# Kernel optimization log

Hardware: AMD Instinct MI355X
Metric: run time of the kernel (lower is better)

Reference implementation:

```python
import jax, jax.numpy as jnp
import numpy as np

N = 50000      # nodes
E = 800000     # directed edges (before self loops)
IN = 64        # in_channels
HID = 96       # hidden_dim
HEADS = 4
C = HID // HEADS
L = 4          # num_layers
G = 1024       # num graphs (molecules)
OUT = 1
BN_EPS = 1e-5


def setup_inputs() -> dict:
    key = jax.random.key(0)
    ks = jax.random.split(key, 20)
    x = jax.random.normal(ks[0], (N, IN), jnp.float32)
    edge_index = jax.random.randint(ks[1], (2, E), 0, N, dtype=jnp.int32)
    batch = jnp.sort(jax.random.randint(ks[2], (N,), 0, G, dtype=jnp.int32))
    def lin(k, fi, fo):
        return jax.random.normal(k, (fi, fo), jnp.float32) / np.sqrt(fi)
    return {
        "x": x, "edge_index": edge_index, "batch": batch,
        "W_in": lin(ks[3], IN, HID), "b_in": jnp.zeros((HID,), jnp.float32),
        "Wg": jax.random.normal(ks[4], (L, HID, HID), jnp.float32) / np.sqrt(HID),
        "att_src": jax.random.normal(ks[5], (L, HEADS, C), jnp.float32) / np.sqrt(C),
        "att_dst": jax.random.normal(ks[6], (L, HEADS, C), jnp.float32) / np.sqrt(C),
        "bg": jnp.zeros((L, HID), jnp.float32),
        "gamma": jnp.ones((L, HID), jnp.float32),
        "beta": jnp.zeros((L, HID), jnp.float32),
        "rm": 0.1 * jax.random.normal(ks[7], (L, HID), jnp.float32),
        "rv": jax.random.uniform(ks[8], (L, HID), jnp.float32, 0.5, 1.5),
        "W_jk": lin(ks[9], HID * L, HID), "b_jk": jnp.zeros((HID,), jnp.float32),
        "W_h1": lin(ks[10], HID, HID), "b_h1": jnp.zeros((HID,), jnp.float32),
        "W_h2": lin(ks[11], HID, OUT), "b_h2": jnp.zeros((OUT,), jnp.float32),
    }


def gat_conv(h_in, src, dst, W, a_s, a_d, b):
    # PyG GATConv (concat=True, negative_slope=0.2), eval mode (no dropout)
    h = (h_in @ W).reshape(N, HEADS, C)                      # [N,H,C]
    e = (h * a_s).sum(-1)[src] + (h * a_d).sum(-1)[dst]      # [E',H]
    e = jax.nn.leaky_relu(e, 0.2)
    m = jax.ops.segment_max(e, dst, num_segments=N)          # segment softmax over dst
    p = jnp.exp(e - m[dst])
    z = jax.ops.segment_sum(p, dst, num_segments=N)
    alpha = p / (z[dst] + 1e-16)                             # [E',H]
    out = jax.ops.segment_sum(h[src] * alpha[:, :, None], dst, num_segments=N)
    return out.reshape(N, HID) + b


def reference(x, edge_index, batch, W_in, b_in, Wg, att_src, att_dst, bg,
              gamma, beta, rm, rv, W_jk, b_jk, W_h1, b_h1, W_h2, b_h2):
    # add self loops (PyG GATConv default)
    loops = jnp.arange(N, dtype=edge_index.dtype)
    src = jnp.concatenate([edge_index[0], loops])
    dst = jnp.concatenate([edge_index[1], loops])

    h = jax.nn.elu(x @ W_in + b_in)
    pooled = []
    for i in range(L):
        hn = gat_conv(h, src, dst, Wg[i], att_src[i], att_dst[i], bg[i])
        hn = (hn - rm[i]) / jnp.sqrt(rv[i] + BN_EPS) * gamma[i] + beta[i]
        h = h + jax.nn.elu(hn)                               # residual
        pooled.append(jax.ops.segment_sum(h, batch, num_segments=G))
    z = jax.nn.elu(jnp.concatenate(pooled, axis=-1) @ W_jk + b_jk)  # JK
    z = jax.nn.relu(z @ W_h1 + b_h1)
    return z @ W_h2 + b_h2                                    # [G, OUT]
```

## Files before the change

kernel.cpp:

```cpp
#include <hip/hip_runtime.h>
#include <hip/hip_bf16.h>
#include <math.h>

#define NODES 50000
#define EDGES 800000
#define EP    850000
#define INCH  64
#define HIDD  96
#define NHEAD 4
#define CHD   24
#define NLAY  4
#define NGRF  1024
#define BNEPS 1e-5f
#define NB    49
#define HSTR  98

__device__ __forceinline__ float elu1(float v) { return v > 0.f ? v : __expf(v) - 1.f; }

__device__ __forceinline__ unsigned short f2bf(float f) {
    unsigned u = __float_as_uint(f);
    return (unsigned short)((u + 0x7fffu + ((u >> 16) & 1u)) >> 16);
}

__device__ __forceinline__ float rl_f(float v, int l) {
    return __int_as_float(__builtin_amdgcn_readlane(__float_as_int(v), l));
}

__device__ __forceinline__ float bnorm(float a, const float* __restrict__ bg,
                                       const float* __restrict__ rm, const float* __restrict__ rv,
                                       const float* __restrict__ gamma, const float* __restrict__ beta,
                                       int ch) {
    float hn = a + bg[ch];
    return (hn - rm[ch]) / sqrtf(rv[ch] + BNEPS) * gamma[ch] + beta[ch];
}

__device__ __forceinline__ void edge_sd(int e, const int* __restrict__ S,
                                        const int* __restrict__ D, int& s, int& d) {
    if (e < EDGES) { s = S[e]; d = D[e]; } else { s = e - EDGES; d = s; }
}


__global__ __launch_bounds__(256) void k_count(const int* __restrict__ S, const int* __restrict__ D,
                                               int* __restrict__ cnt) {
    int e = blockIdx.x * blockDim.x + threadIdx.x;
    if (e >= EP) return;
    int s, d; edge_sd(e, S, D, s, d);
    atomicAdd(&cnt[d], 1);
}

__global__ __launch_bounds__(1024) void k_scan1(const int* __restrict__ cnt,
                                                int* __restrict__ off, int* __restrict__ bsum) {
    __shared__ int sd[1024];
    int t = threadIdx.x;
    int i = blockIdx.x * 1024 + t;
    int v = (i < NODES) ? cnt[i] : 0;
    sd[t] = v; __syncthreads();
    for (int o = 1; o < 1024; o <<= 1) {
        int tv = (t >= o) ? sd[t - o] : 0;
        __syncthreads();
        sd[t] += tv; __syncthreads();
    }
    if (i < NODES) off[i] = sd[t] - v;
    if (t == 1023) bsum[blockIdx.x] = sd[1023];
}

__global__ __launch_bounds__(1024) void k_scan3m(int* __restrict__ off, const int* __restrict__ bsum,
                                                 int* __restrict__ cursor) {
    int carry = 0;
    for (int b = 0; b < blockIdx.x; ++b) carry += bsum[b];
    int i = blockIdx.x * 1024 + threadIdx.x;
    if (i < NODES) {
        int o = off[i] + carry;
        off[i] = o;
        cursor[i] = o;
    }
    if (i == 0) off[NODES] = EP;
}

__global__ __launch_bounds__(256) void k_scatter(const int* __restrict__ S, const int* __restrict__ D,
                                                 int* __restrict__ cursor, int* __restrict__ csr_src) {
    int e = blockIdx.x * blockDim.x + threadIdx.x;
    if (e >= EP) return;
    int s, d; edge_sd(e, S, D, s, d);
    int pos = atomicAdd(&cursor[d], 1);
    csr_src[pos] = s;
}


__global__ __launch_bounds__(256) void k_in_proj_proj(const float* __restrict__ x,
                                                      const float* __restrict__ W_in,
                                                      const float* __restrict__ b_in,
                                                      const float* __restrict__ Wg0,
                                                      const float* __restrict__ asrc,
                                                      const float* __restrict__ adst,
                                                      float* __restrict__ h,
                                                      unsigned* __restrict__ hpb,
                                                      float* __restrict__ as_,
                                                      float* __restrict__ ad_) {
    __shared__ float Wl[HIDD * HIDD];
    __shared__ float hblk[64 * HSTR];
    int tid = threadIdx.x;
    for (int i = tid; i < INCH * HIDD / 4; i += 256)
        ((float4*)Wl)[i] = ((const float4*)W_in)[i];
    __syncthreads();

    int lane = tid & 63;
    int node = blockIdx.x * 64 + lane;
    bool valid = node < NODES;
    int head = tid >> 6;
    int cbase = head * CHD;

    {
        const float* __restrict__ xr = x + (size_t)node * INCH;
        float acc[CHD];
#pragma unroll
        for (int j = 0; j < CHD; ++j) acc[j] = b_in[cbase + j];
        if (valid) {
            for (int k0 = 0; k0 < INCH; k0 += 4) {
                float4 xv = *(const float4*)(xr + k0);
                const float xvv[4] = {xv.x, xv.y, xv.z, xv.w};
#pragma unroll
                for (int kk = 0; kk < 4; ++kk) {
#pragma unroll
                    for (int j4 = 0; j4 < CHD; j4 += 4) {
                        float4 wv = *(const float4*)(&Wl[(k0 + kk) * HIDD + cbase + j4]);
                        acc[j4 + 0] = fmaf(xvv[kk], wv.x, acc[j4 + 0]);
                        acc[j4 + 1] = fmaf(xvv[kk], wv.y, acc[j4 + 1]);
                        acc[j4 + 2] = fmaf(xvv[kk], wv.z, acc[j4 + 2]);
                        acc[j4 + 3] = fmaf(xvv[kk], wv.w, acc[j4 + 3]);
                    }
                }
            }
        }
        float* hrow = h + (size_t)node * HIDD + cbase;
#pragma unroll
        for (int j = 0; j < CHD; ++j) {
            float hv = elu1(acc[j]);
            hblk[lane * HSTR + cbase + j] = hv;
            if (valid) hrow[j] = hv;
        }
    }
    __syncthreads();
    for (int i = tid; i < HIDD * HIDD / 4; i += 256)
        ((float4*)Wl)[i] = ((const float4*)Wg0)[i];
    __syncthreads();

    const float* __restrict__ hr = &hblk[lane * HSTR];
    float acc[CHD] = {};
    for (int k0 = 0; k0 < HIDD; k0 += 2) {
        float2 hv = *(const float2*)(hr + k0);
        const float hvv[2] = {hv.x, hv.y};
#pragma unroll
        for (int kk = 0; kk < 2; ++kk) {
#pragma unroll
            for (int j4 = 0; j4 < CHD; j4 += 4) {
                float4 wv = *(const float4*)(&Wl[(k0 + kk) * HIDD + cbase + j4]);
                acc[j4 + 0] = fmaf(hvv[kk], wv.x, acc[j4 + 0]);
                acc[j4 + 1] = fmaf(hvv[kk], wv.y, acc[j4 + 1]);
                acc[j4 + 2] = fmaf(hvv[kk], wv.z, acc[j4 + 2]);
                acc[j4 + 3] = fmaf(hvv[kk], wv.w, acc[j4 + 3]);
            }
        }
    }
    if (valid) {
        unsigned* orow = hpb + (size_t)node * (HIDD / 2) + cbase / 2;
#pragma unroll
        for (int j = 0; j < CHD; j += 2)
            orow[j / 2] = (unsigned)f2bf(acc[j]) | ((unsigned)f2bf(acc[j + 1]) << 16);
        const float* __restrict__ s = asrc + head * CHD;
        const float* __restrict__ d = adst + head * CHD;
        float sa = 0.f, da = 0.f;
#pragma unroll
        for (int j = 0; j < CHD; ++j) { sa = fmaf(acc[j], s[j], sa); da = fmaf(acc[j], d[j], da); }
        as_[node * NHEAD + head] = sa;
        ad_[node * NHEAD + head] = da;
    }
}


__global__ __launch_bounds__(256) void k_proj(const float* __restrict__ h,
                                              const float* __restrict__ W,
                                              const float* __restrict__ asrc,
                                              const float* __restrict__ adst,
                                              unsigned* __restrict__ hpb,
                                              float* __restrict__ as_,
                                              float* __restrict__ ad_) {
    __shared__ float Wl[HIDD * HIDD];
    int tid = threadIdx.x;
    for (int i = tid; i < HIDD * HIDD / 4; i += 256)
        ((float4*)Wl)[i] = ((const float4*)W)[i];
    __syncthreads();

    int node = blockIdx.x * 64 + (tid & 63);
    if (node >= NODES) return;
    int head = tid >> 6;
    int cbase = head * CHD;
    const float* __restrict__ hr = h + (size_t)node * HIDD;

    float acc[CHD] = {};
    for (int k0 = 0; k0 < HIDD; k0 += 4) {
        float4 hv = *(const float4*)(hr + k0);
        const float hvv[4] = {hv.x, hv.y, hv.z, hv.w};
#pragma unroll
        for (int kk = 0; kk < 4; ++kk) {
#pragma unroll
            for (int j4 = 0; j4 < CHD; j4 += 4) {
                float4 wv = *(const float4*)(&Wl[(k0 + kk) * HIDD + cbase + j4]);
                acc[j4 + 0] = fmaf(hvv[kk], wv.x, acc[j4 + 0]);
                acc[j4 + 1] = fmaf(hvv[kk], wv.y, acc[j4 + 1]);
                acc[j4 + 2] = fmaf(hvv[kk], wv.z, acc[j4 + 2]);
                acc[j4 + 3] = fmaf(hvv[kk], wv.w, acc[j4 + 3]);
            }
        }
    }
    unsigned* orow = hpb + (size_t)node * (HIDD / 2) + cbase / 2;
#pragma unroll
    for (int j = 0; j < CHD; j += 2)
        orow[j / 2] = (unsigned)f2bf(acc[j]) | ((unsigned)f2bf(acc[j + 1]) << 16);

    const float* __restrict__ s = asrc + head * CHD;
    const float* __restrict__ d = adst + head * CHD;
    float sa = 0.f, da = 0.f;
#pragma unroll
    for (int j = 0; j < CHD; ++j) { sa = fmaf(acc[j], s[j], sa); da = fmaf(acc[j], d[j], da); }
    as_[node * NHEAD + head] = sa;
    ad_[node * NHEAD + head] = da;
}


__global__ __launch_bounds__(256) void k_edge(const int* __restrict__ off,
                                              const int* __restrict__ csr,
                                              const float* __restrict__ as_,
                                              const float* __restrict__ ad_,
                                              const unsigned* __restrict__ hpb,
                                              const float* __restrict__ bg,
                                              const float* __restrict__ gamma,
                                              const float* __restrict__ beta,
                                              const float* __restrict__ rm,
                                              const float* __restrict__ rv,
                                              float* __restrict__ h,
                                              const int* __restrict__ batch,
                                              float* __restrict__ pooled) {
    __shared__ float plds[512];
    int tid = threadIdx.x;
    int lane = tid & 63;
    int n0 = __builtin_amdgcn_readfirstlane(blockIdx.x * 8 + (tid >> 6) * 2);
    int n1 = n0 + 1;
    int beg0 = off[n0], end0 = off[n0 + 1], end1 = off[n0 + 2];
    int beg1 = end0;

    int hd = lane & 3, slot = lane >> 2;
    float adv0 = ad_[n0 * NHEAD + hd];
    float adv1 = ad_[n1 * NHEAD + hd];
    const int hh = (lane < 48) ? (lane / 12) : 0;
    const bool gl = (lane < 48);
    const int wb = (tid & 192) * 2;

    float a00 = 0.f, a01 = 0.f, a10 = 0.f, a11 = 0.f, zA = 0.f, zB = 0.f;
    int ca = beg0, cb = beg1;
    while (ca < end0 || cb < end1) {
        int cntA = min(16, end0 - ca);
        int cntB = min(16, end1 - cb);
        int sA = 0, sB = 0;
        if (cntA > 0) {
            int i = ca + slot, ii = min(i, end0 - 1);
            sA = csr[ii];
            float ev = as_[sA * NHEAD + hd] + adv0;
            ev = ev > 0.f ? ev : 0.2f * ev;
            float p = (i < end0) ? __expf(ev) : 0.f;
            zA += p;
            plds[wb + lane] = p;
        }
        if (cntB > 0) {
            int i = cb + slot, ii = min(i, end1 - 1);
            sB = csr[ii];
            float ev = as_[sB * NHEAD + hd] + adv1;
            ev = ev > 0.f ? ev : 0.2f * ev;
            float p = (i < end1) ? __expf(ev) : 0.f;
            zB += p;
            plds[wb + 64 + lane] = p;
        }
        if (cntA > 0) {
#pragma unroll
            for (int j = 0; j < 16; ++j) {
                if (j < cntA) {
                    int sv = __builtin_amdgcn_readlane(sA, j * 4);
                    float al = plds[wb + j * 4 + hh];
                    if (gl) {
                        unsigned u = (hpb + (size_t)sv * (HIDD / 2))[lane];
                        a00 = fmaf(__uint_as_float(u << 16),         al, a00);
                        a01 = fmaf(__uint_as_float(u & 0xffff0000u), al, a01);
                    }
                }
            }
            ca += 16;
        }
        if (cntB > 0) {
#pragma unroll
            for (int j = 0; j < 16; ++j) {
                if (j < cntB) {
                    int sv = __builtin_amdgcn_readlane(sB, j * 4);
                    float al = plds[wb + 64 + j * 4 + hh];
                    if (gl) {
                        unsigned u = (hpb + (size_t)sv * (HIDD / 2))[lane];
                        a10 = fmaf(__uint_as_float(u << 16),         al, a10);
                        a11 = fmaf(__uint_as_float(u & 0xffff0000u), al, a11);
                    }
                }
            }
            cb += 16;
        }
    }
#pragma unroll
    for (int o = 4; o < 64; o <<= 1) { zA += __shfl_xor(zA, o); zB += __shfl_xor(zB, o); }
    float za0 = rl_f(zA, 0), za1 = rl_f(zA, 1), za2 = rl_f(zA, 2), za3 = rl_f(zA, 3);
    float zb0 = rl_f(zB, 0), zb1 = rl_f(zB, 1), zb2 = rl_f(zB, 2), zb3 = rl_f(zB, 3);
    float zAl = (hh & 1) ? za1 : za0, zAh = (hh & 1) ? za3 : za2;
    float zBl = (hh & 1) ? zb1 : zb0, zBh = (hh & 1) ? zb3 : zb2;
    float zhA = (hh & 2) ? zAh : zAl;
    float zhB = (hh & 2) ? zBh : zBl;

    int g0 = batch[n0], g1 = batch[n1];
    if (gl) {
        float izA = 1.f / zhA, izB = 1.f / zhB;
        a00 *= izA; a01 *= izA; a10 *= izB; a11 *= izB;
        int ch0 = 2 * lane, ch1 = ch0 + 1;
        float hn00 = bnorm(a00, bg, rm, rv, gamma, beta, ch0);
        float hn01 = bnorm(a01, bg, rm, rv, gamma, beta, ch1);
        float hn10 = bnorm(a10, bg, rm, rv, gamma, beta, ch0);
        float hn11 = bnorm(a11, bg, rm, rv, gamma, beta, ch1);
        float2 hv0 = *(float2*)(h + (size_t)n0 * HIDD + ch0);
        float2 hv1 = *(float2*)(h + (size_t)n1 * HIDD + ch0);
        hv0.x += elu1(hn00); hv0.y += elu1(hn01);
        hv1.x += elu1(hn10); hv1.y += elu1(hn11);
        *(float2*)(h + (size_t)n0 * HIDD + ch0) = hv0;
        *(float2*)(h + (size_t)n1 * HIDD + ch0) = hv1;
        if (g0 == g1) {
            atomicAdd(&pooled[g0 * HIDD + ch0], hv0.x + hv1.x);
            atomicAdd(&pooled[g0 * HIDD + ch1], hv0.y + hv1.y);
        } else {
            atomicAdd(&pooled[g0 * HIDD + ch0], hv0.x);
            atomicAdd(&pooled[g0 * HIDD + ch1], hv0.y);
            atomicAdd(&pooled[g1 * HIDD + ch0], hv1.x);
            atomicAdd(&pooled[g1 * HIDD + ch1], hv1.y);
        }
    }
}


__global__ __launch_bounds__(128) void k_head(const float* __restrict__ pooled,
                                              const float* __restrict__ Wjk, const float* __restrict__ bjk,
                                              const float* __restrict__ Wh1, const float* __restrict__ bh1,
                                              const float* __restrict__ Wh2, const float* __restrict__ bh2,
                                              float* __restrict__ out) {
    __shared__ float pin[NLAY * HIDD];
    __shared__ float z1[HIDD];
    __shared__ float z2[HIDD];
    int g = blockIdx.x, tid = threadIdx.x;
    for (int idx = tid; idx < NLAY * HIDD; idx += blockDim.x) {
        int l = idx / HIDD, c = idx % HIDD;
        pin[idx] = pooled[(size_t)l * NGRF * HIDD + (size_t)g * HIDD + c];
    }
    __syncthreads();
    for (int c = tid; c < HIDD; c += blockDim.x) {
        float a = bjk[c];
        for (int k = 0; k < NLAY * HIDD; ++k) a = fmaf(pin[k], Wjk[k * HIDD + c], a);
        z1[c] = elu1(a);
    }
    __syncthreads();
    for (int c = tid; c < HIDD; c += blockDim.x) {
        float a = bh1[c];
#pragma unroll
        for (int k = 0; k < HIDD; ++k) a = fmaf(z1[k], Wh1[k * HIDD + c], a);
        z2[c] = fmaxf(a, 0.f);
    }
    __syncthreads();
    if (tid < 64) {
        float a = 0.f;
        for (int k = tid; k < HIDD; k += 64) a = fmaf(z2[k], Wh2[k], a);
#pragma unroll
        for (int o = 32; o > 0; o >>= 1) a += __shfl_down(a, o);
        if (tid == 0) out[g] = a + bh2[0];
    }
}

extern "C" void kernel_launch(void* const* d_in, const int* in_sizes, int n_in,
                              void* d_out, int out_size, void* d_ws, size_t ws_size,
                              hipStream_t stream) {
    const float* x     = (const float*)d_in[0];
    const int*   ei    = (const int*)d_in[1];
    const int*   batch = (const int*)d_in[2];
    const float* W_in  = (const float*)d_in[3];
    const float* b_in  = (const float*)d_in[4];
    const float* Wg    = (const float*)d_in[5];
    const float* att_s = (const float*)d_in[6];
    const float* att_d = (const float*)d_in[7];
    const float* bg    = (const float*)d_in[8];
    const float* gamma = (const float*)d_in[9];
    const float* beta  = (const float*)d_in[10];
    const float* rm    = (const float*)d_in[11];
    const float* rv    = (const float*)d_in[12];
    const float* Wjk   = (const float*)d_in[13];
    const float* bjk   = (const float*)d_in[14];
    const float* Wh1   = (const float*)d_in[15];
    const float* bh1   = (const float*)d_in[16];
    const float* Wh2   = (const float*)d_in[17];
    const float* bh2   = (const float*)d_in[18];
    float* out = (float*)d_out;

    const int* S = ei;
    const int* Dd = ei + EDGES;

    float* ws = (float*)d_ws;
    float*    h      = ws;
    float*    as_    = h    + (size_t)NODES * HIDD;
    float*    ad_    = as_  + (size_t)NODES * NHEAD;
    float*    pooled = ad_  + (size_t)NODES * NHEAD;
    unsigned* hpb    = (unsigned*)(pooled + (size_t)NLAY * NGRF * HIDD);
    int*      off    = (int*)(hpb + (size_t)NODES * (HIDD / 2));
    int*      cursor = off    + NODES + 2;
    int*      csr    = cursor + NODES;
    int*      cnt    = csr    + EP;
    int*      bsum   = cnt    + NODES;

    hipMemsetAsync(pooled, 0, sizeof(float) * NLAY * NGRF * HIDD, stream);
    hipMemsetAsync(cnt, 0, sizeof(int) * NODES, stream);

    const int TB = 256;
    int gE    = (EP + TB - 1) / TB;
    int gTile = (NODES + 63) / 64;
    int gEdge = NODES / 8;

    k_count<<<gE, TB, 0, stream>>>(S, Dd, cnt);
    k_scan1<<<NB, 1024, 0, stream>>>(cnt, off, bsum);
    k_scan3m<<<NB, 1024, 0, stream>>>(off, bsum, cursor);
    k_scatter<<<gE, TB, 0, stream>>>(S, Dd, cursor, csr);

    k_in_proj_proj<<<gTile, TB, 0, stream>>>(x, W_in, b_in, Wg, att_s, att_d,
                                             h, hpb, as_, ad_);
    k_edge<<<gEdge, TB, 0, stream>>>(off, csr, as_, ad_, hpb,
                                     bg, gamma, beta, rm, rv, h, batch, pooled);

    for (int i = 1; i < NLAY; ++i) {
        k_proj<<<gTile, TB, 0, stream>>>(h, Wg + (size_t)i * HIDD * HIDD,
                                         att_s + i * NHEAD * CHD, att_d + i * NHEAD * CHD,
                                         hpb, as_, ad_);
        k_edge<<<gEdge, TB, 0, stream>>>(off, csr, as_, ad_, hpb,
                                         bg + i * HIDD, gamma + i * HIDD, beta + i * HIDD,
                                         rm + i * HIDD, rv + i * HIDD, h, batch,
                                         pooled + (size_t)i * NGRF * HIDD);
    }

    k_head<<<NGRF, 128, 0, stream>>>(pooled, Wjk, bjk, Wh1, bh1, Wh2, bh2, out);
}
```

Baseline: 553.3 us.

## Batch edge gathers before FMAs, drop LDS staging, fold pooled zeroing into kernel

In the edge aggregation loop, all 16 bf16 row gathers and alpha values for both destination nodes are now loaded into register arrays before any FMA, instead of interleaving each load with its FMA. The aim is more loads in flight to hide gather latency. The input-projection kernel no longer stages h in LDS: it reads h back from global memory with float4 loads, and it zeroes the pooled buffer itself, which replaces a separate memset. The head kernel gets unroll-8 pragmas. The extra register arrays can raise VGPR pressure and lower occupancy. The global read-back of h relies on block-level visibility after __syncthreads.

```diff
diff --git a/kernel.cpp b/kernel.cpp
--- a/kernel.cpp
+++ b/kernel.cpp
@@ -13,7 +13,6 @@
 #define NGRF  1024
 #define BNEPS 1e-5f
 #define NB    49
-#define HSTR  98
 
 __device__ __forceinline__ float elu1(float v) { return v > 0.f ? v : __expf(v) - 1.f; }
 
@@ -96,10 +95,13 @@
                                                       float* __restrict__ h,
                                                       unsigned* __restrict__ hpb,
                                                       float* __restrict__ as_,
-                                                      float* __restrict__ ad_) {
+                                                      float* __restrict__ ad_,
+                                                      float* __restrict__ pooled_all) {
     __shared__ float Wl[HIDD * HIDD];
-    __shared__ float hblk[64 * HSTR];
     int tid = threadIdx.x;
+    for (size_t i = (size_t)blockIdx.x * 256 + tid; i < (size_t)NLAY * NGRF * HIDD;
+         i += (size_t)gridDim.x * 256)
+        pooled_all[i] = 0.f;
     for (int i = tid; i < INCH * HIDD / 4; i += 256)
         ((float4*)Wl)[i] = ((const float4*)W_in)[i];
     __syncthreads();
@@ -131,13 +133,9 @@
                     }
                 }
             }
-        }
-        float* hrow = h + (size_t)node * HIDD + cbase;
-#pragma unroll
-        for (int j = 0; j < CHD; ++j) {
-            float hv = elu1(acc[j]);
-            hblk[lane * HSTR + cbase + j] = hv;
-            if (valid) hrow[j] = hv;
+            float* hrow = h + (size_t)node * HIDD + cbase;
+#pragma unroll
+            for (int j = 0; j < CHD; ++j) hrow[j] = elu1(acc[j]);
         }
     }
     __syncthreads();
@@ -145,13 +143,13 @@
         ((float4*)Wl)[i] = ((const float4*)Wg0)[i];
     __syncthreads();
 
-    const float* __restrict__ hr = &hblk[lane * HSTR];
+    const float* __restrict__ hr = h + (size_t)node * HIDD;
     float acc[CHD] = {};
-    for (int k0 = 0; k0 < HIDD; k0 += 2) {
-        float2 hv = *(const float2*)(hr + k0);
-        const float hvv[2] = {hv.x, hv.y};
-#pragma unroll
-        for (int kk = 0; kk < 2; ++kk) {
+    for (int k0 = 0; k0 < HIDD; k0 += 4) {
+        float4 hv = *(const float4*)(hr + k0);
+        const float hvv[4] = {hv.x, hv.y, hv.z, hv.w};
+#pragma unroll
+        for (int kk = 0; kk < 4; ++kk) {
 #pragma unroll
             for (int j4 = 0; j4 < CHD; j4 += 4) {
                 float4 wv = *(const float4*)(&Wl[(k0 + kk) * HIDD + cbase + j4]);
@@ -280,36 +278,40 @@
             zB += p;
             plds[wb + 64 + lane] = p;
         }
-        if (cntA > 0) {
-#pragma unroll
-            for (int j = 0; j < 16; ++j) {
-                if (j < cntA) {
-                    int sv = __builtin_amdgcn_readlane(sA, j * 4);
-                    float al = plds[wb + j * 4 + hh];
-                    if (gl) {
-                        unsigned u = (hpb + (size_t)sv * (HIDD / 2))[lane];
-                        a00 = fmaf(__uint_as_float(u << 16),         al, a00);
-                        a01 = fmaf(__uint_as_float(u & 0xffff0000u), al, a01);
-                    }
-                }
-            }
-            ca += 16;
-        }
-        if (cntB > 0) {
-#pragma unroll
-            for (int j = 0; j < 16; ++j) {
-                if (j < cntB) {
-                    int sv = __builtin_amdgcn_readlane(sB, j * 4);
-                    float al = plds[wb + 64 + j * 4 + hh];
-                    if (gl) {
-                        unsigned u = (hpb + (size_t)sv * (HIDD / 2))[lane];
-                        a10 = fmaf(__uint_as_float(u << 16),         al, a10);
-                        a11 = fmaf(__uint_as_float(u & 0xffff0000u), al, a11);
-                    }
-                }
-            }
-            cb += 16;
-        }
+        unsigned uA[16], uB[16];
+        float alA[16], alB[16];
+#pragma unroll
+        for (int j = 0; j < 16; ++j) {
+            if (j < cntA) {
+                int sv = __builtin_amdgcn_readlane(sA, j * 4);
+                alA[j] = plds[wb + j * 4 + hh];
+                if (gl) uA[j] = (hpb + (size_t)sv * (HIDD / 2))[lane];
+            }
+        }
+#pragma unroll
+        for (int j = 0; j < 16; ++j) {
+            if (j < cntB) {
+                int sv = __builtin_amdgcn_readlane(sB, j * 4);
+                alB[j] = plds[wb + 64 + j * 4 + hh];
+                if (gl) uB[j] = (hpb + (size_t)sv * (HIDD / 2))[lane];
+            }
+        }
+#pragma unroll
+        for (int j = 0; j < 16; ++j) {
+            if (j < cntA && gl) {
+                a00 = fmaf(__uint_as_float(uA[j] << 16),         alA[j], a00);
+                a01 = fmaf(__uint_as_float(uA[j] & 0xffff0000u), alA[j], a01);
+            }
+        }
+#pragma unroll
+        for (int j = 0; j < 16; ++j) {
+            if (j < cntB && gl) {
+                a10 = fmaf(__uint_as_float(uB[j] << 16),         alB[j], a10);
+                a11 = fmaf(__uint_as_float(uB[j] & 0xffff0000u), alB[j], a11);
+            }
+        }
+        if (cntA > 0) ca += 16;
+        if (cntB > 0) cb += 16;
     }
 #pragma unroll
     for (int o = 4; o < 64; o <<= 1) { zA += __shfl_xor(zA, o); zB += __shfl_xor(zB, o); }
@@ -364,13 +366,14 @@
     __syncthreads();
     for (int c = tid; c < HIDD; c += blockDim.x) {
         float a = bjk[c];
+#pragma unroll 8
         for (int k = 0; k < NLAY * HIDD; ++k) a = fmaf(pin[k], Wjk[k * HIDD + c], a);
         z1[c] = elu1(a);
     }
     __syncthreads();
     for (int c = tid; c < HIDD; c += blockDim.x) {
         float a = bh1[c];
-#pragma unroll
+#pragma unroll 8
         for (int k = 0; k < HIDD; ++k) a = fmaf(z1[k], Wh1[k * HIDD + c], a);
         z2[c] = fmaxf(a, 0.f);
     }
@@ -423,7 +426,6 @@
     int*      cnt    = csr    + EP;
     int*      bsum   = cnt    + NODES;
 
-    hipMemsetAsync(pooled, 0, sizeof(float) * NLAY * NGRF * HIDD, stream);
     hipMemsetAsync(cnt, 0, sizeof(int) * NODES, stream);
 
     const int TB = 256;
@@ -437,7 +439,7 @@
     k_scatter<<<gE, TB, 0, stream>>>(S, Dd, cursor, csr);
 
     k_in_proj_proj<<<gTile, TB, 0, stream>>>(x, W_in, b_in, Wg, att_s, att_d,
-                                             h, hpb, as_, ad_);
+                                             h, hpb, as_, ad_, pooled);
     k_edge<<<gEdge, TB, 0, stream>>>(off, csr, as_, ad_, hpb,
                                      bg, gamma, beta, rm, rv, h, batch, pooled);
 
```

After: 641.2 us. 1.16x slower.
